# Kernel tuning notes

Hardware: AMD Instinct MI355X
Metric: run time of the kernel (lower is better)

The kernel has to match this reference:

```python
import jax, jax.numpy as jnp
import numpy as np

D_MODEL = 1024
D_STATE = 16
D_CONV = 4
EXPAND = 2
D_INNER = EXPAND * D_MODEL          # 2048
DT_RANK = (D_MODEL + 15) // 16      # 64 (mamba default 'auto')
B_SZ = 4
SEQ = 2048
EPS = 1e-12


def setup_inputs() -> dict:
    key = jax.random.key(0)
    ks = jax.random.split(key, 12)
    s = 0.02
    n = lambda k, sh: (jax.random.normal(k, sh, jnp.float32) * s)
    A_log = jnp.log(jnp.broadcast_to(
        jnp.arange(1, D_STATE + 1, dtype=jnp.float32), (D_INNER, D_STATE)))
    return {
        "input_tensor": jax.random.normal(ks[0], (B_SZ, SEQ, D_MODEL), jnp.float32),
        "in_proj_w": n(ks[1], (2 * D_INNER, D_MODEL)),
        "conv_w": n(ks[2], (D_INNER, D_CONV)),
        "conv_b": n(ks[3], (D_INNER,)),
        "x_proj_w": n(ks[4], (DT_RANK + 2 * D_STATE, D_INNER)),
        "dt_proj_w": n(ks[5], (D_INNER, DT_RANK)),
        "dt_proj_b": jax.random.uniform(ks[6], (D_INNER,), jnp.float32, -4.0, -2.0),
        "A_log": A_log,
        "D": jnp.ones((D_INNER,), jnp.float32),
        "out_proj_w": n(ks[7], (D_MODEL, D_INNER)),
        "norm_w": jnp.ones((D_MODEL,), jnp.float32),
        "ffn_w1": n(ks[8], (4 * D_MODEL, D_MODEL)),
        "ffn_b1": jnp.zeros((4 * D_MODEL,), jnp.float32),
        "ffn_w2": n(ks[9], (D_MODEL, 4 * D_MODEL)),
        "ffn_b2": jnp.zeros((D_MODEL,), jnp.float32),
        "ffn_norm_w": jnp.ones((D_MODEL,), jnp.float32),
    }


def rmsnorm(x, w, eps=EPS):
    return x * jax.lax.rsqrt(jnp.mean(x * x, axis=-1, keepdims=True) + eps) * w


def causal_dwconv(x, w, b):
    # x: (B, L, D); w: (D, K) depthwise causal conv, output length L
    xc = jnp.swapaxes(x, 1, 2)  # (B, D, L)
    out = jax.lax.conv_general_dilated(
        xc, w[:, None, :], window_strides=(1,),
        padding=[(w.shape[1] - 1, 0)],
        dimension_numbers=("NCH", "OIH", "NCH"),
        feature_group_count=w.shape[0])
    return jnp.swapaxes(out, 1, 2) + b


def selective_scan(u, delta, A, Bm, Cm):
    # u, delta: (B, L, D); Bm, Cm: (B, L, N); A: (D, N)
    def step(h, inp):
        d_t, u_t, b_t, c_t = inp           # (B,D), (B,D), (B,N), (B,N)
        dA = jnp.exp(d_t[..., None] * A)   # (B, D, N)
        h = dA * h + (d_t * u_t)[..., None] * b_t[:, None, :]
        y = jnp.einsum("bdn,bn->bd", h, c_t)
        return h, y
    h0 = jnp.zeros((u.shape[0], u.shape[2], A.shape[1]), u.dtype)
    xs = (jnp.swapaxes(delta, 0, 1), jnp.swapaxes(u, 0, 1),
          jnp.swapaxes(Bm, 0, 1), jnp.swapaxes(Cm, 0, 1))
    _, ys = jax.lax.scan(step, h0, xs)     # ys: (L, B, D)
    return jnp.swapaxes(ys, 0, 1)


def mamba_block(x, in_proj_w, conv_w, conv_b, x_proj_w, dt_proj_w, dt_proj_b,
                A_log, D, out_proj_w):
    xz = x @ in_proj_w.T                    # (B, L, 2*D_INNER)
    u, z = jnp.split(xz, 2, axis=-1)
    u = jax.nn.silu(causal_dwconv(u, conv_w, conv_b))
    x_dbl = u @ x_proj_w.T                  # (B, L, dt_rank + 2*N)
    dt = x_dbl[..., :DT_RANK]
    Bm = x_dbl[..., DT_RANK:DT_RANK + D_STATE]
    Cm = x_dbl[..., DT_RANK + D_STATE:]
    delta = jax.nn.softplus(dt @ dt_proj_w.T + dt_proj_b)
    A = -jnp.exp(A_log)
    y = selective_scan(u, delta, A, Bm, Cm) + u * D
    y = y * jax.nn.silu(z)
    return y @ out_proj_w.T


def reference(input_tensor, in_proj_w, conv_w, conv_b, x_proj_w, dt_proj_w,
              dt_proj_b, A_log, D, out_proj_w, norm_w, ffn_w1, ffn_b1,
              ffn_w2, ffn_b2, ffn_norm_w):
    h = mamba_block(input_tensor, in_proj_w, conv_w, conv_b, x_proj_w,
                    dt_proj_w, dt_proj_b, A_log, D, out_proj_w)
    # num_blocks=2 -> residual; dropout is identity at eval
    h = rmsnorm(h + input_tensor, norm_w)
    ff = jax.nn.gelu(h @ ffn_w1.T + ffn_b1, approximate=False) @ ffn_w2.T + ffn_b2
    return rmsnorm(ff + h, ffn_norm_w)
```

## Files before the change

kernel.cpp:

```cpp
#include <hip/hip_runtime.h>
#include <cstdint>
#include <cstddef>

#define SEQ    2048
#define NB     4
#define DM     1024
#define DI     2048
#define MTOK   (NB*SEQ)
#define NCHUNK 32
#define TCH    64

typedef unsigned short u16;
typedef __attribute__((ext_vector_type(8))) short  short8;
typedef __attribute__((ext_vector_type(4))) float  f32x4;
typedef __attribute__((ext_vector_type(4))) unsigned short us4;

__device__ __forceinline__ float b2f(u16 u){ union{unsigned i; float f;} c; c.i=((unsigned)u)<<16; return c.f; }
__device__ __forceinline__ u16 f2b(float f){
  union{float f; unsigned u;} c; c.f=f;
  unsigned r = c.u + 0x7fffu + ((c.u>>16)&1u);
  return (u16)(r>>16);
}

__device__ __forceinline__ void gload_lds16(const void* g, void* l){
  __builtin_amdgcn_global_load_lds((const __attribute__((address_space(1))) void*)g,
                                   (__attribute__((address_space(3))) void*)l, 16, 0, 0);
}

__global__ __launch_bounds__(256) void cvt_k(const float* __restrict__ in,
                                             u16* __restrict__ out, int n8){
  const int i = blockIdx.x*256 + threadIdx.x;
  if (i >= n8) return;
  const f32x4 a = ((const f32x4*)in)[2*i];
  const f32x4 b = ((const f32x4*)in)[2*i+1];
  short8 r;
  #pragma unroll
  for (int e=0;e<4;e++){ r[e] = (short)f2b(a[e]); r[e+4] = (short)f2b(b[e]); }
  ((short8*)out)[i] = r;
}

__global__ __launch_bounds__(256) void padcvt_k(const float* __restrict__ in,
                                                u16* __restrict__ out){
  const int i = blockIdx.x*256 + threadIdx.x;
  const int row = (i*8) >> 11;
  short8 r;
  if (row < 96){
    const f32x4 a = ((const f32x4*)in)[2*i];
    const f32x4 b = ((const f32x4*)in)[2*i+1];
    #pragma unroll
    for (int e=0;e<4;e++){ r[e] = (short)f2b(a[e]); r[e+4] = (short)f2b(b[e]); }
  } else {
    #pragma unroll
    for (int e=0;e<8;e++) r[e] = 0;
  }
  ((short8*)out)[i] = r;
}

template<int MW, int EPI>
__global__ __launch_bounds__(512, 2) void gemm8(
    const u16* __restrict__ X, int lda,
    const u16* __restrict__ W,
    const float* __restrict__ bias,
    void* __restrict__ Cout,
    int N, int K, int gridX)
{
  constexpr int BM = 128*MW;
  __shared__ __align__(16) u16 As[2][MW][128*64];
  __shared__ __align__(16) u16 Bs[2][2][128*64];

  const int nwg  = gridDim.x;
  const int orig = blockIdx.x;
  const int swz  = (orig & 7)*(nwg >> 3) + (orig >> 3);
  const int bm0  = (swz / gridX) * BM;
  const int bn0  = (swz % gridX) * 256;

  const int tid  = threadIdx.x;
  const int lane = tid & 63;
  const int wv   = tid >> 6;
  const int wm   = wv >> 2;
  const int wn   = wv & 3;

  const int trow = tid >> 3;
  const int sl   = tid & 7;
  const int scol = (sl ^ (trow & 7)) << 3;

  const u16* gA = X + (size_t)bm0*lda + scol;
  const u16* gB = W + (size_t)bn0*K   + scol;
  const int nk = K >> 6;

  auto stageA = [&](int slot, int unit, int tile){
    if (tile < nk){
      const int kt = tile << 6;
      #pragma unroll
      for (int l=0;l<2;l++){
        const int hrow = l*64 + trow;
        gload_lds16(gA + (size_t)(unit*128 + hrow)*lda + kt,
                    &As[slot][unit][hrow*64 + sl*8]);
      }
    }
  };
  auto stageB = [&](int slot, int half, int tile){
    if (tile < nk){
      const int kt = tile << 6;
      #pragma unroll
      for (int l=0;l<2;l++){
        const int hrow = l*64 + trow;
        gload_lds16(gB + (size_t)(half*128 + hrow)*K + kt,
                    &Bs[slot][half][hrow*64 + sl*8]);
      }
    }
  };

  f32x4 acc[4][MW][4];
  #pragma unroll
  for (int p=0;p<4;p++)
    #pragma unroll
    for (int i=0;i<MW;i++)
      #pragma unroll
      for (int j=0;j<4;j++){ f32x4 z={0.f,0.f,0.f,0.f}; acc[p][i][j]=z; }

  const int lrow = lane & 15;
  const int lhi  = lane >> 4;
  const int r7   = lane & 7;

  stageB(0,0,0); stageB(0,1,0);
  stageA(0,0,0); if constexpr (MW==2) stageA(0,1,0);
  stageB(1,0,1); stageB(1,1,1);
  if constexpr (MW==2) stageA(1,0,1);
  if constexpr (MW==2) asm volatile("s_waitcnt vmcnt(6)":::"memory");
  else                 asm volatile("s_waitcnt vmcnt(4)":::"memory");
  __builtin_amdgcn_s_barrier();

  for (int T0 = 0; T0 < nk; T0 += 2) {
    #pragma unroll
    for (int sub = 0; sub < 2; ++sub) {
      const int T = T0 + sub;
      short8 bf[4][2];
      #pragma unroll
      for (int p = 0; p < 4; ++p) {
        if (p == 0) {
          #pragma unroll
          for (int j=0;j<4;j++){
            const int gn = wn*64 + j*16 + lrow;
            const int bh = gn >> 7, br = gn & 127;
            #pragma unroll
            for (int ks=0;ks<2;ks++){
              const int s8 = ((ks<<2)|lhi) ^ r7;
              bf[j][ks] = *(const short8*)&Bs[sub][bh][br*64 + s8*8];
            }
          }
        }
        short8 af[MW][2];
        #pragma unroll
        for (int i=0;i<MW;i++){
          const int gm = (2*p + wm)*(16*MW) + i*16 + lrow;
          const int ah = (MW==2) ? (gm >> 7) : 0;
          const int ar = gm & 127;
          #pragma unroll
          for (int ks=0;ks<2;ks++){
            const int s8 = ((ks<<2)|lhi) ^ r7;
            af[i][ks] = *(const short8*)&As[sub][ah][ar*64 + s8*8];
          }
        }
        if (p == 0)      stageA(sub^1, MW-1, T+1);
        else if (p == 1) stageB(sub, 0, T+2);
        else if (p == 2) stageB(sub, 1, T+2);
        else if constexpr (MW==2) { if (p == 3) stageA(sub, 0, T+2); }
        if (p == 3 && T+1 < nk) {
          if (T+2 < nk) {
            if constexpr (MW==2) asm volatile("s_waitcnt vmcnt(6)":::"memory");
            else                 asm volatile("s_waitcnt vmcnt(4)":::"memory");
          } else {
            asm volatile("s_waitcnt vmcnt(0)":::"memory");
          }
        }
        __builtin_amdgcn_s_barrier();
        asm volatile("s_waitcnt lgkmcnt(0)":::"memory");
        __builtin_amdgcn_s_setprio(1);
        #pragma unroll
        for (int ks=0;ks<2;ks++)
          #pragma unroll
          for (int i=0;i<MW;i++)
            #pragma unroll
            for (int j=0;j<4;j++)
              acc[p][i][j] = __builtin_amdgcn_mfma_f32_16x16x32_bf16(af[i][ks], bf[j][ks], acc[p][i][j], 0, 0, 0);
        __builtin_amdgcn_s_setprio(0);
        __builtin_amdgcn_s_barrier();
      }
    }
  }

  const int r0 = (lane >> 4) << 2;
  #pragma unroll
  for (int p=0;p<4;p++){
    #pragma unroll
    for (int i=0;i<MW;i++){
      #pragma unroll
      for (int j=0;j<4;j++){
        const int col = bn0 + wn*64 + j*16 + lrow;
        float bval = 0.f;
        if constexpr (EPI >= 2) bval = bias[col];
        #pragma unroll
        for (int r=0;r<4;r++){
          const int row = bm0 + (2*p + wm)*(16*MW) + i*16 + r0 + r;
          const float v = acc[p][i][j][r];
          const size_t oid = (size_t)row*N + col;
          if constexpr (EPI == 0) {
            ((u16*)Cout)[oid] = f2b(v);
          } else if constexpr (EPI == 1) {
            ((float*)Cout)[oid] = v;
          } else if constexpr (EPI == 2) {
            float xv = v + bval;
            float sp = (xv > 20.f) ? xv : log1pf(__expf(xv));
            ((u16*)Cout)[oid] = f2b(sp);
          } else if constexpr (EPI == 3) {
            float xv = v + bval;
            float g = 0.5f*xv*(1.f + erff(xv*0.70710678118f));
            ((u16*)Cout)[oid] = f2b(g);
          } else {
            ((float*)Cout)[oid] = v + bval;
          }
        }
      }
    }
  }
}

template<int EPI>
__global__ __launch_bounds__(256) void gemm_bt(
    const u16* __restrict__ X, int lda,
    const u16* __restrict__ W,
    const float* __restrict__ bias,
    void* __restrict__ Cout,
    int M, int N, int K)
{
  __shared__ __align__(16) u16 As[128*64];
  __shared__ __align__(16) u16 Bs[128*64];
  const int tid  = threadIdx.x;
  const int lane = tid & 63;
  const int wv   = tid >> 6;
  const int wr   = wv >> 1, wc = wv & 1;
  const int bm0  = blockIdx.y * 128;
  const int bn0  = blockIdx.x * 128;
  const int r0   = tid >> 3;
  const int c8   = (tid & 7) << 3;

  f32x4 acc[4][4];
  #pragma unroll
  for (int i=0;i<4;i++)
    #pragma unroll
    for (int j=0;j<4;j++){ f32x4 z = {0.f,0.f,0.f,0.f}; acc[i][j] = z; }

  const int lrow = lane & 15;
  const int lko  = (lane >> 4) << 3;

  for (int kt = 0; kt < K; kt += 64) {
    #pragma unroll
    for (int c = 0; c < 4; ++c) {
      const int row = c*32 + r0;
      gload_lds16(X + (size_t)(bm0+row)*lda + kt + c8, &As[row*64 + c8]);
      gload_lds16(W + (size_t)(bn0+row)*K   + kt + c8, &Bs[row*64 + c8]);
    }
    __syncthreads();
    #pragma unroll
    for (int kk = 0; kk < 2; ++kk) {
      short8 af[4], bf[4];
      #pragma unroll
      for (int i=0;i<4;i++) af[i] = *(const short8*)&As[(wr*64 + i*16 + lrow)*64 + kk*32 + lko];
      #pragma unroll
      for (int j=0;j<4;j++) bf[j] = *(const short8*)&Bs[(wc*64 + j*16 + lrow)*64 + kk*32 + lko];
      #pragma unroll
      for (int i=0;i<4;i++)
        #pragma unroll
        for (int j=0;j<4;j++)
          acc[i][j] = __builtin_amdgcn_mfma_f32_16x16x32_bf16(af[i], bf[j], acc[i][j], 0, 0, 0);
    }
    __syncthreads();
  }

  const int rbase = bm0 + wr*64 + ((lane>>4)<<2);
  const int cbase = bn0 + wc*64 + (lane & 15);
  #pragma unroll
  for (int i=0;i<4;i++) {
    #pragma unroll
    for (int j=0;j<4;j++) {
      const int col = cbase + j*16;
      float bval = 0.f;
      if constexpr (EPI >= 2) bval = bias[col];
      #pragma unroll
      for (int r=0;r<4;r++) {
        const int row = rbase + i*16 + r;
        const float v = acc[i][j][r];
        const size_t oid = (size_t)row*N + col;
        if constexpr (EPI == 0) {
          ((u16*)Cout)[oid] = f2b(v);
        } else if constexpr (EPI == 1) {
          ((float*)Cout)[oid] = v;
        } else if constexpr (EPI == 2) {
          float xv = v + bval;
          float sp = (xv > 20.f) ? xv : log1pf(__expf(xv));
          ((u16*)Cout)[oid] = f2b(sp);
        } else if constexpr (EPI == 3) {
          float xv = v + bval;
          float g = 0.5f*xv*(1.f + erff(xv*0.70710678118f));
          ((u16*)Cout)[oid] = f2b(g);
        } else {
          ((float*)Cout)[oid] = v + bval;
        }
      }
    }
  }
}

__global__ __launch_bounds__(256) void gemm_thin(
    const u16* __restrict__ X, int lda,
    const u16* __restrict__ W,
    u16* __restrict__ Cout, int K)
{
  __shared__ __align__(16) u16 As[32*64];
  __shared__ __align__(16) u16 Bs[128*64];
  const int tid  = threadIdx.x;
  const int lane = tid & 63;
  const int wvq  = tid >> 6;
  const int bm0  = blockIdx.x * 32;
  const int srow = tid >> 3;
  const int c8   = (tid & 7) << 3;

  f32x4 acc[2][2];
  #pragma unroll
  for (int i=0;i<2;i++)
    #pragma unroll
    for (int j=0;j<2;j++){ f32x4 z={0.f,0.f,0.f,0.f}; acc[i][j]=z; }

  const int lrow = lane & 15;
  const int lko  = (lane >> 4) << 3;

  for (int kt = 0; kt < K; kt += 64) {
    gload_lds16(X + (size_t)(bm0+srow)*lda + kt + c8, &As[srow*64 + c8]);
    #pragma unroll
    for (int c=0;c<4;c++){
      const int row = c*32 + srow;
      gload_lds16(W + (size_t)row*K + kt + c8, &Bs[row*64 + c8]);
    }
    __syncthreads();
    #pragma unroll
    for (int ks=0;ks<2;ks++){
      short8 af[2], bf[2];
      #pragma unroll
      for (int i=0;i<2;i++) af[i] = *(const short8*)&As[(i*16+lrow)*64 + ks*32 + lko];
      #pragma unroll
      for (int j=0;j<2;j++) bf[j] = *(const short8*)&Bs[(wvq*32 + j*16 + lrow)*64 + ks*32 + lko];
      #pragma unroll
      for (int i=0;i<2;i++)
        #pragma unroll
        for (int j=0;j<2;j++)
          acc[i][j] = __builtin_amdgcn_mfma_f32_16x16x32_bf16(af[i], bf[j], acc[i][j], 0, 0, 0);
    }
    __syncthreads();
  }

  const int r0 = (lane >> 4) << 2;
  #pragma unroll
  for (int i=0;i<2;i++)
    #pragma unroll
    for (int j=0;j<2;j++){
      const int col = wvq*32 + j*16 + lrow;
      #pragma unroll
      for (int r=0;r<4;r++){
        const int row = bm0 + i*16 + r0 + r;
        Cout[(size_t)row*128 + col] = f2b(acc[i][j][r]);
      }
    }
}

__global__ __launch_bounds__(256) void conv_silu_k(
    const u16* __restrict__ xz, const float* __restrict__ cw,
    const float* __restrict__ cb, u16* __restrict__ uout)
{
  const int m0 = blockIdx.x << 2;
  const int t0 = m0 & (SEQ-1);
  const int d8 = threadIdx.x << 3;
  float w[4][8];
  const float* wp = cw + (size_t)d8*4;
  #pragma unroll
  for (int q=0;q<8;q++){
    f32x4 v = ((const f32x4*)wp)[q];
    #pragma unroll
    for (int e=0;e<4;e++){ int li=q*4+e; w[li&3][li>>2]=v[e]; }
  }
  float bias[8];
  {
    f32x4 b0 = ((const f32x4*)&cb[d8])[0];
    f32x4 b1 = ((const f32x4*)&cb[d8])[1];
    #pragma unroll
    for (int e=0;e<4;e++){ bias[e]=b0[e]; bias[e+4]=b1[e]; }
  }
  float xv[7][8];
  #pragma unroll
  for (int r=0;r<7;r++){
    const int t = t0 - 3 + r;
    if (t >= 0){
      short8 v = *(const short8*)&xz[(size_t)(m0-3+r)*4096 + d8];
      #pragma unroll
      for (int e=0;e<8;e++) xv[r][e] = b2f((u16)v[e]);
    } else {
      #pragma unroll
      for (int e=0;e<8;e++) xv[r][e] = 0.f;
    }
  }
  #pragma unroll
  for (int q=0;q<4;q++){
    short8 r8;
    #pragma unroll
    for (int e=0;e<8;e++){
      float a = bias[e];
      #pragma unroll
      for (int j=0;j<4;j++) a = fmaf(xv[q+j][e], w[j][e], a);
      r8[e] = (short)f2b(a / (1.f + __expf(-a)));
    }
    *(short8*)&uout[(size_t)(m0+q)*2048 + d8] = r8;
  }
}

template<int PASS>
__global__ __launch_bounds__(256) void scan_chunk_k(
    u16* __restrict__ dly,
    const u16* __restrict__ ucv,
    const u16* __restrict__ xz,
    const u16* __restrict__ xdbl,
    const float* __restrict__ A_log,
    const float* __restrict__ Dp,
    float* __restrict__ summ)
{
  __shared__ __align__(16) u16 sBC [TCH*32];
  __shared__ __align__(16) u16 sDel[16*256];
  __shared__ __align__(16) u16 sU  [16*256];
  __shared__ __align__(16) u16 sZ  [16*256];

  const int tid   = threadIdx.x;
  const int chgrp = blockIdx.x;
  const int chunk = blockIdx.y;
  const int ch    = chgrp*256 + tid;
  const int b     = ch >> 11;
  const int d     = ch & (DI-1);
  const int t0    = chunk*TCH;
  const int dbase = (chgrp & 7) << 8;

  float A[16];
  #pragma unroll
  for (int n=0;n<16;n++) A[n] = -__expf(A_log[d*16 + n]);

  {
    const int row = tid >> 2, q8 = (tid & 3) << 3;
    *(short8*)&sBC[row*32 + q8] =
      *(const short8*)&xdbl[((size_t)(b*SEQ) + t0 + row)*128 + 64 + q8];
  }

  float h[16];
  if constexpr (PASS == 1) {
    #pragma unroll
    for (int n=0;n<16;n++) h[n] = 0.f;
  } else {
    #pragma unroll
    for (int n=0;n<16;n++) h[n] = summ[((size_t)(chunk*17 + n))*8192 + ch];
  }
  float S = 0.f;
  float Dd = 0.f;
  if constexpr (PASS == 3) Dd = Dp[d];

  const int srow = tid >> 5;
  const int scol = (tid & 31) << 3;
  const size_t gD = (size_t)(b*SEQ)*DI   + dbase + scol;
  const size_t gZ = (size_t)(b*SEQ)*4096 + 2048 + dbase + scol;

  short8 pD[2], pU[2], pZ[2];
  #pragma unroll
  for (int k=0;k<2;k++){
    const size_t tg = (size_t)(t0 + k*8 + srow);
    pD[k] = *(const short8*)&dly[gD + tg*DI];
    pU[k] = *(const short8*)&ucv[gD + tg*DI];
    if constexpr (PASS == 3) pZ[k] = *(const short8*)&xz[gZ + tg*4096];
  }

  for (int sc = 0; sc < TCH/16; ++sc) {
    __syncthreads();
    #pragma unroll
    for (int k=0;k<2;k++){
      *(short8*)&sDel[(k*8+srow)*256 + scol] = pD[k];
      *(short8*)&sU  [(k*8+srow)*256 + scol] = pU[k];
      if constexpr (PASS == 3) *(short8*)&sZ[(k*8+srow)*256 + scol] = pZ[k];
    }
    if (sc < TCH/16 - 1) {
      #pragma unroll
      for (int k=0;k<2;k++){
        const size_t tg = (size_t)(t0 + (sc+1)*16 + k*8 + srow);
        pD[k] = *(const short8*)&dly[gD + tg*DI];
        pU[k] = *(const short8*)&ucv[gD + tg*DI];
        if constexpr (PASS == 3) pZ[k] = *(const short8*)&xz[gZ + tg*4096];
      }
    }
    __syncthreads();

    #pragma unroll 2
    for (int j=0; j<16; ++j){
      const int r = sc*16 + j;
      const float del = b2f(sDel[j*256 + tid]);
      const float u   = b2f(sU  [j*256 + tid]);
      const float du  = del * u;
      if constexpr (PASS == 1) S += del;
      const short8 bv0 = *(const short8*)&sBC[r*32];
      const short8 bv1 = *(const short8*)&sBC[r*32 + 8];
      short8 cv0, cv1;
      if constexpr (PASS == 3){
        cv0 = *(const short8*)&sBC[r*32 + 16];
        cv1 = *(const short8*)&sBC[r*32 + 24];
      }
      float p0=0.f, p1=0.f, p2=0.f, p3=0.f;
      #pragma unroll
      for (int n=0;n<16;++n){
        const float Bn = b2f((u16)(n<8 ? bv0[n] : bv1[n-8]));
        const float eA = __expf(del * A[n]);
        h[n] = fmaf(eA, h[n], du * Bn);
        if constexpr (PASS == 3){
          const float Cn = b2f((u16)(n<8 ? cv0[n] : cv1[n-8]));
          if      ((n&3)==0) p0 = fmaf(h[n], Cn, p0);
          else if ((n&3)==1) p1 = fmaf(h[n], Cn, p1);
          else if ((n&3)==2) p2 = fmaf(h[n], Cn, p2);
          else               p3 = fmaf(h[n], Cn, p3);
        }
      }
      if constexpr (PASS == 3){
        const float p = (p0+p1)+(p2+p3);
        const float z = b2f(sZ[j*256 + tid]);
        float y = fmaf(u, Dd, p);
        y *= z / (1.f + __expf(-z));
        dly[(size_t)(b*SEQ + t0 + r)*DI + d] = f2b(y);
      }
    }
  }

  if constexpr (PASS == 1){
    #pragma unroll
    for (int n=0;n<16;n++) summ[((size_t)(chunk*17 + n))*8192 + ch] = h[n];
    summ[((size_t)(chunk*17 + 16))*8192 + ch] = S;
  }
}

__global__ __launch_bounds__(256) void scan_combine_k(
    float* __restrict__ summ, const float* __restrict__ A_log)
{
  const int ch = blockIdx.x*256 + threadIdx.x;
  const int d  = ch & (DI-1);
  float A[16];
  #pragma unroll
  for (int n=0;n<16;n++) A[n] = -__expf(A_log[d*16 + n]);
  float hi[16];
  #pragma unroll
  for (int n=0;n<16;n++) hi[n] = 0.f;
  for (int c=0; c<NCHUNK; ++c){
    float hf[16]; float Sc = 0.f;
    if (c < NCHUNK-1) {
      #pragma unroll
      for (int n=0;n<16;n++) hf[n] = summ[((size_t)(c*17 + n))*8192 + ch];
      Sc = summ[((size_t)(c*17 + 16))*8192 + ch];
    }
    #pragma unroll
    for (int n=0;n<16;n++) summ[((size_t)(c*17 + n))*8192 + ch] = hi[n];
    if (c < NCHUNK-1) {
      #pragma unroll
      for (int n=0;n<16;n++) hi[n] = fmaf(__expf(A[n]*Sc), hi[n], hf[n]);
    }
  }
}

template<bool RES_BF, bool OUT_BF>
__global__ __launch_bounds__(256) void add_rms_k(
    const float* __restrict__ a, const void* __restrict__ res,
    const float* __restrict__ wgt, void* __restrict__ out)
{
  const int row = blockIdx.x;
  const int tid = threadIdx.x;
  const size_t base = (size_t)row*DM + tid*4;
  const f32x4 av = *(const f32x4*)&a[base];
  const f32x4 wv = *(const f32x4*)&wgt[tid*4];
  float v[4]; float ss = 0.f;
  if constexpr (RES_BF) {
    const us4 rv = *(const us4*)&((const u16*)res)[base];
    #pragma unroll
    for (int j=0;j<4;j++){ v[j] = av[j] + b2f(rv[j]); ss = fmaf(v[j], v[j], ss); }
  } else {
    const f32x4 rv = *(const f32x4*)&((const float*)res)[base];
    #pragma unroll
    for (int j=0;j<4;j++){ v[j] = av[j] + rv[j]; ss = fmaf(v[j], v[j], ss); }
  }
  #pragma unroll
  for (int off=32; off>=1; off>>=1) ss += __shfl_xor(ss, off);
  __shared__ float sred[4];
  if ((tid & 63) == 0) sred[tid>>6] = ss;
  __syncthreads();
  const float tot = sred[0]+sred[1]+sred[2]+sred[3];
  const float rs = rsqrtf(tot * (1.f/1024.f) + 1e-12f);
  if constexpr (OUT_BF) {
    us4 ov;
    #pragma unroll
    for (int j=0;j<4;j++) ov[j] = (unsigned short)f2b(v[j] * rs * wv[j]);
    *(us4*)&((u16*)out)[base] = ov;
  } else {
    f32x4 ov;
    #pragma unroll
    for (int j=0;j<4;j++) ov[j] = v[j] * rs * wv[j];
    *(f32x4*)&((float*)out)[base] = ov;
  }
}

extern "C" void kernel_launch(void* const* d_in, const int* in_sizes, int n_in,
                              void* d_out, int out_size, void* d_ws, size_t ws_size,
                              hipStream_t stream) {
  (void)in_sizes; (void)n_in; (void)out_size; (void)ws_size;
  const float* x_in  = (const float*)d_in[0];
  const float* w_inp = (const float*)d_in[1];
  const float* conv_w= (const float*)d_in[2];
  const float* conv_b= (const float*)d_in[3];
  const float* w_xp  = (const float*)d_in[4];
  const float* w_dt  = (const float*)d_in[5];
  const float* b_dt  = (const float*)d_in[6];
  const float* A_log = (const float*)d_in[7];
  const float* Dp    = (const float*)d_in[8];
  const float* w_out = (const float*)d_in[9];
  const float* norm_w= (const float*)d_in[10];
  const float* w_f1  = (const float*)d_in[11];
  const float* b_f1  = (const float*)d_in[12];
  const float* w_f2  = (const float*)d_in[13];
  const float* b_f2  = (const float*)d_in[14];
  const float* norm2 = (const float*)d_in[15];

  char* ws = (char*)d_ws;
  size_t off = 0;
  auto alloc = [&](size_t bytes){ void* p = ws + off; off += (bytes + 255) & ~255ull; return p; };
  u16*   xz   = (u16*)  alloc((size_t)MTOK*4096*2);
  u16*   ucv  = (u16*)  alloc((size_t)MTOK*2048*2);
  u16*   xdbl = (u16*)  alloc((size_t)MTOK*128*2);
  u16*   dly  = (u16*)  alloc((size_t)MTOK*2048*2);
  float* tmp  = (float*)alloc((size_t)MTOK*1024*4);
  u16*   wA   = (u16*)  alloc((size_t)4096*1024*2);
  u16*   wpad = (u16*)  alloc((size_t)128*2048*2);
  u16*   wdt  = (u16*)  alloc((size_t)2048*64*2);
  u16*   wout = (u16*)  alloc((size_t)1024*2048*2);
  u16*   xbf  = (u16*)tmp;
  float* summ = tmp;
  u16*   hbuf = ucv;

  cvt_k<<<4096, 256, 0, stream>>>(x_in,  xbf, MTOK*DM/8);
  cvt_k<<<2048, 256, 0, stream>>>(w_inp, wA,  (2*DI*DM)/8);
  padcvt_k<<<128, 256, 0, stream>>>(w_xp, wpad);
  cvt_k<<<64,   256, 0, stream>>>(w_dt,  wdt, (DI*64)/8);
  cvt_k<<<1024, 256, 0, stream>>>(w_out, wout,(DM*DI)/8);

  gemm8<2,0><<<512, 512, 0, stream>>>(xbf, 1024, wA, nullptr, xz, 4096, 1024, 16);
  conv_silu_k<<<MTOK/4, 256, 0, stream>>>(xz, conv_w, conv_b, ucv);
  gemm_thin<<<256, 256, 0, stream>>>(ucv, 2048, wpad, xdbl, 2048);
  gemm_bt<2><<<dim3(16,64), 256, 0, stream>>>(xdbl, 128, wdt, b_dt, dly, MTOK, 2048, 64);
  scan_chunk_k<1><<<dim3(32, NCHUNK-1), 256, 0, stream>>>(dly, ucv, xz, xdbl, A_log, Dp, summ);
  scan_combine_k<<<32, 256, 0, stream>>>(summ, A_log);
  scan_chunk_k<3><<<dim3(32, NCHUNK), 256, 0, stream>>>(dly, ucv, xz, xdbl, A_log, Dp, summ);
  gemm8<1,1><<<256, 512, 0, stream>>>(dly, 2048, wout, nullptr, tmp, 1024, 2048, 4);
  add_rms_k<false,true><<<MTOK, 256, 0, stream>>>(tmp, x_in, norm_w, hbuf);
  cvt_k<<<2048, 256, 0, stream>>>(w_f1, wA, (4*DM*DM)/8);
  gemm8<2,3><<<512, 512, 0, stream>>>(hbuf, 1024, wA, b_f1, xz, 4096, 1024, 16);
  cvt_k<<<2048, 256, 0, stream>>>(w_f2, wA, (4*DM*DM)/8);
  gemm8<1,4><<<256, 512, 0, stream>>>(xz, 4096, wA, b_f2, tmp, 1024, 4096, 4);
  add_rms_k<true,false><<<MTOK, 256, 0, stream>>>(tmp, hbuf, norm2, d_out);
}
```

Measured before the change: 622.5 us.

## Replace large 8-wave GEMM with simpler 128x128 double-buffered GEMM; merge conversion kernels

Replaces the 256x256/128x256 tile, 512-thread GEMM, which had a fine-grained interleaved prefetch schedule, with a 128x128 tile, 256-thread kernel that uses plain double buffering and one barrier pair per k-tile. It also fuses the five fp32-to-bf16 conversion launches into one kernel that dispatches on block index. The simpler GEMM launches more blocks with smaller tiles, which cuts per-block register and LDS pressure. In exchange each tile gets less data reuse and there is more global/LDS traffic per FLOP, and the loss of the tuned overlap schedule risks lower MFMA utilisation.

```diff
diff --git a/kernel.cpp b/kernel.cpp
--- a/kernel.cpp
+++ b/kernel.cpp
@@ -27,6 +27,44 @@
                                    (__attribute__((address_space(3))) void*)l, 16, 0, 0);
 }
 
+__global__ __launch_bounds__(256) void mega_cvt(
+    const float* __restrict__ x,    const float* __restrict__ winp,
+    const float* __restrict__ wxp,  const float* __restrict__ wdt_,
+    const float* __restrict__ wout_,
+    u16* __restrict__ xbf, u16* __restrict__ wA, u16* __restrict__ wpadb,
+    u16* __restrict__ wdtb, u16* __restrict__ woutb)
+{
+  const int b = blockIdx.x;
+  const int t = threadIdx.x;
+  const float* src; u16* dst; int i;
+  if (b < 4096)      { i = b*256 + t;        src = x;     dst = xbf;  }
+  else if (b < 6144) { i = (b-4096)*256 + t; src = winp;  dst = wA;   }
+  else if (b < 6272) {
+    i = (b-6144)*256 + t;
+    const int row = (i*8) >> 11;
+    short8 r;
+    if (row < 96){
+      const f32x4 a = ((const f32x4*)wxp)[2*i];
+      const f32x4 c = ((const f32x4*)wxp)[2*i+1];
+      #pragma unroll
+      for (int e=0;e<4;e++){ r[e]=(short)f2b(a[e]); r[e+4]=(short)f2b(c[e]); }
+    } else {
+      #pragma unroll
+      for (int e=0;e<8;e++) r[e]=0;
+    }
+    ((short8*)wpadb)[i] = r;
+    return;
+  }
+  else if (b < 6336) { i = (b-6272)*256 + t; src = wdt_;  dst = wdtb; }
+  else               { i = (b-6336)*256 + t; src = wout_; dst = woutb;}
+  const f32x4 a = ((const f32x4*)src)[2*i];
+  const f32x4 c = ((const f32x4*)src)[2*i+1];
+  short8 r;
+  #pragma unroll
+  for (int e=0;e<4;e++){ r[e]=(short)f2b(a[e]); r[e+4]=(short)f2b(c[e]); }
+  ((short8*)dst)[i] = r;
+}
+
 __global__ __launch_bounds__(256) void cvt_k(const float* __restrict__ in,
                                              u16* __restrict__ out, int n8){
   const int i = blockIdx.x*256 + threadIdx.x;
@@ -39,46 +77,27 @@
   ((short8*)out)[i] = r;
 }
 
-__global__ __launch_bounds__(256) void padcvt_k(const float* __restrict__ in,
-                                                u16* __restrict__ out){
-  const int i = blockIdx.x*256 + threadIdx.x;
-  const int row = (i*8) >> 11;
-  short8 r;
-  if (row < 96){
-    const f32x4 a = ((const f32x4*)in)[2*i];
-    const f32x4 b = ((const f32x4*)in)[2*i+1];
-    #pragma unroll
-    for (int e=0;e<4;e++){ r[e] = (short)f2b(a[e]); r[e+4] = (short)f2b(b[e]); }
-  } else {
-    #pragma unroll
-    for (int e=0;e<8;e++) r[e] = 0;
-  }
-  ((short8*)out)[i] = r;
-}
-
-template<int MW, int EPI>
-__global__ __launch_bounds__(512, 2) void gemm8(
+template<int EPI>
+__global__ __launch_bounds__(256, 2) void gemm_db(
     const u16* __restrict__ X, int lda,
     const u16* __restrict__ W,
     const float* __restrict__ bias,
     void* __restrict__ Cout,
     int N, int K, int gridX)
 {
-  constexpr int BM = 128*MW;
-  __shared__ __align__(16) u16 As[2][MW][128*64];
-  __shared__ __align__(16) u16 Bs[2][2][128*64];
+  __shared__ __align__(16) u16 Ab[2][128*64];
+  __shared__ __align__(16) u16 Bb[2][128*64];
 
   const int nwg  = gridDim.x;
   const int orig = blockIdx.x;
   const int swz  = (orig & 7)*(nwg >> 3) + (orig >> 3);
-  const int bm0  = (swz / gridX) * BM;
-  const int bn0  = (swz % gridX) * 256;
+  const int bm0  = (swz / gridX) * 128;
+  const int bn0  = (swz % gridX) * 128;
 
   const int tid  = threadIdx.x;
   const int lane = tid & 63;
   const int wv   = tid >> 6;
-  const int wm   = wv >> 2;
-  const int wn   = wv & 3;
+  const int wr   = wv >> 1, wc = wv & 1;
 
   const int trow = tid >> 3;
   const int sl   = tid & 7;
@@ -88,138 +107,88 @@
   const u16* gB = W + (size_t)bn0*K   + scol;
   const int nk = K >> 6;
 
-  auto stageA = [&](int slot, int unit, int tile){
-    if (tile < nk){
-      const int kt = tile << 6;
-      #pragma unroll
-      for (int l=0;l<2;l++){
-        const int hrow = l*64 + trow;
-        gload_lds16(gA + (size_t)(unit*128 + hrow)*lda + kt,
-                    &As[slot][unit][hrow*64 + sl*8]);
-      }
+  auto stage = [&](int buf, int tile){
+    const int kt = tile << 6;
+    #pragma unroll
+    for (int g=0; g<4; ++g){
+      const int row = g*32 + trow;
+      gload_lds16(gA + (size_t)row*lda + kt, &Ab[buf][row*64 + sl*8]);
+    }
+    #pragma unroll
+    for (int g=0; g<4; ++g){
+      const int row = g*32 + trow;
+      gload_lds16(gB + (size_t)row*K + kt, &Bb[buf][row*64 + sl*8]);
     }
   };
-  auto stageB = [&](int slot, int half, int tile){
-    if (tile < nk){
-      const int kt = tile << 6;
-      #pragma unroll
-      for (int l=0;l<2;l++){
-        const int hrow = l*64 + trow;
-        gload_lds16(gB + (size_t)(half*128 + hrow)*K + kt,
-                    &Bs[slot][half][hrow*64 + sl*8]);
-      }
-    }
-  };
-
-  f32x4 acc[4][MW][4];
-  #pragma unroll
-  for (int p=0;p<4;p++)
-    #pragma unroll
-    for (int i=0;i<MW;i++)
-      #pragma unroll
-      for (int j=0;j<4;j++){ f32x4 z={0.f,0.f,0.f,0.f}; acc[p][i][j]=z; }
+
+  f32x4 acc[4][4];
+  #pragma unroll
+  for (int i=0;i<4;i++)
+    #pragma unroll
+    for (int j=0;j<4;j++){ f32x4 z={0.f,0.f,0.f,0.f}; acc[i][j]=z; }
 
   const int lrow = lane & 15;
   const int lhi  = lane >> 4;
   const int r7   = lane & 7;
 
-  stageB(0,0,0); stageB(0,1,0);
-  stageA(0,0,0); if constexpr (MW==2) stageA(0,1,0);
-  stageB(1,0,1); stageB(1,1,1);
-  if constexpr (MW==2) stageA(1,0,1);
-  if constexpr (MW==2) asm volatile("s_waitcnt vmcnt(6)":::"memory");
-  else                 asm volatile("s_waitcnt vmcnt(4)":::"memory");
-  __builtin_amdgcn_s_barrier();
-
-  for (int T0 = 0; T0 < nk; T0 += 2) {
-    #pragma unroll
-    for (int sub = 0; sub < 2; ++sub) {
-      const int T = T0 + sub;
-      short8 bf[4][2];
-      #pragma unroll
-      for (int p = 0; p < 4; ++p) {
-        if (p == 0) {
-          #pragma unroll
-          for (int j=0;j<4;j++){
-            const int gn = wn*64 + j*16 + lrow;
-            const int bh = gn >> 7, br = gn & 127;
-            #pragma unroll
-            for (int ks=0;ks<2;ks++){
-              const int s8 = ((ks<<2)|lhi) ^ r7;
-              bf[j][ks] = *(const short8*)&Bs[sub][bh][br*64 + s8*8];
-            }
-          }
-        }
-        short8 af[MW][2];
+  stage(0, 0);
+  stage(1, 1);
+
+  for (int t = 0; t < nk; ++t) {
+    if (t + 1 < nk) asm volatile("s_waitcnt vmcnt(8)":::"memory");
+    else            asm volatile("s_waitcnt vmcnt(0)":::"memory");
+    __builtin_amdgcn_s_barrier();
+    {
+      const u16* As = Ab[t&1];
+      const u16* Bs = Bb[t&1];
+      #pragma unroll
+      for (int ks=0; ks<2; ++ks){
+        const int s8 = ((ks<<2)|lhi) ^ r7;
+        short8 af[4], bf[4];
         #pragma unroll
-        for (int i=0;i<MW;i++){
-          const int gm = (2*p + wm)*(16*MW) + i*16 + lrow;
-          const int ah = (MW==2) ? (gm >> 7) : 0;
-          const int ar = gm & 127;
-          #pragma unroll
-          for (int ks=0;ks<2;ks++){
-            const int s8 = ((ks<<2)|lhi) ^ r7;
-            af[i][ks] = *(const short8*)&As[sub][ah][ar*64 + s8*8];
-          }
-        }
-        if (p == 0)      stageA(sub^1, MW-1, T+1);
-        else if (p == 1) stageB(sub, 0, T+2);
-        else if (p == 2) stageB(sub, 1, T+2);
-        else if constexpr (MW==2) { if (p == 3) stageA(sub, 0, T+2); }
-        if (p == 3 && T+1 < nk) {
-          if (T+2 < nk) {
-            if constexpr (MW==2) asm volatile("s_waitcnt vmcnt(6)":::"memory");
-            else                 asm volatile("s_waitcnt vmcnt(4)":::"memory");
-          } else {
-            asm volatile("s_waitcnt vmcnt(0)":::"memory");
-          }
-        }
-        __builtin_amdgcn_s_barrier();
-        asm volatile("s_waitcnt lgkmcnt(0)":::"memory");
+        for (int i=0;i<4;i++) af[i] = *(const short8*)&As[(wr*64 + i*16 + lrow)*64 + s8*8];
+        #pragma unroll
+        for (int j=0;j<4;j++) bf[j] = *(const short8*)&Bs[(wc*64 + j*16 + lrow)*64 + s8*8];
         __builtin_amdgcn_s_setprio(1);
         #pragma unroll
-        for (int ks=0;ks<2;ks++)
+        for (int i=0;i<4;i++)
           #pragma unroll
-          for (int i=0;i<MW;i++)
-            #pragma unroll
-            for (int j=0;j<4;j++)
-              acc[p][i][j] = __builtin_amdgcn_mfma_f32_16x16x32_bf16(af[i][ks], bf[j][ks], acc[p][i][j], 0, 0, 0);
+          for (int j=0;j<4;j++)
+            acc[i][j] = __builtin_amdgcn_mfma_f32_16x16x32_bf16(af[i], bf[j], acc[i][j], 0, 0, 0);
         __builtin_amdgcn_s_setprio(0);
-        __builtin_amdgcn_s_barrier();
-      }
-    }
+      }
+    }
+    __builtin_amdgcn_s_barrier();
+    if (t + 2 < nk) stage(t&1, t+2);
   }
 
   const int r0 = (lane >> 4) << 2;
   #pragma unroll
-  for (int p=0;p<4;p++){
-    #pragma unroll
-    for (int i=0;i<MW;i++){
-      #pragma unroll
-      for (int j=0;j<4;j++){
-        const int col = bn0 + wn*64 + j*16 + lrow;
-        float bval = 0.f;
-        if constexpr (EPI >= 2) bval = bias[col];
-        #pragma unroll
-        for (int r=0;r<4;r++){
-          const int row = bm0 + (2*p + wm)*(16*MW) + i*16 + r0 + r;
-          const float v = acc[p][i][j][r];
-          const size_t oid = (size_t)row*N + col;
-          if constexpr (EPI == 0) {
-            ((u16*)Cout)[oid] = f2b(v);
-          } else if constexpr (EPI == 1) {
-            ((float*)Cout)[oid] = v;
-          } else if constexpr (EPI == 2) {
-            float xv = v + bval;
-            float sp = (xv > 20.f) ? xv : log1pf(__expf(xv));
-            ((u16*)Cout)[oid] = f2b(sp);
-          } else if constexpr (EPI == 3) {
-            float xv = v + bval;
-            float g = 0.5f*xv*(1.f + erff(xv*0.70710678118f));
-            ((u16*)Cout)[oid] = f2b(g);
-          } else {
-            ((float*)Cout)[oid] = v + bval;
-          }
+  for (int i=0;i<4;i++){
+    #pragma unroll
+    for (int j=0;j<4;j++){
+      const int col = bn0 + wc*64 + j*16 + lrow;
+      float bval = 0.f;
+      if constexpr (EPI >= 2) bval = bias[col];
+      #pragma unroll
+      for (int r=0;r<4;r++){
+        const int row = bm0 + wr*64 + i*16 + r0 + r;
+        const float v = acc[i][j][r];
+        const size_t oid = (size_t)row*N + col;
+        if constexpr (EPI == 0) {
+          ((u16*)Cout)[oid] = f2b(v);
+        } else if constexpr (EPI == 1) {
+          ((float*)Cout)[oid] = v;
+        } else if constexpr (EPI == 2) {
+          float xv = v + bval;
+          float sp = (xv > 20.f) ? xv : log1pf(__expf(xv));
+          ((u16*)Cout)[oid] = f2b(sp);
+        } else if constexpr (EPI == 3) {
+          float xv = v + bval;
+          float g = 0.5f*xv*(1.f + erff(xv*0.70710678118f));
+          ((u16*)Cout)[oid] = f2b(g);
+        } else {
+          ((float*)Cout)[oid] = v + bval;
         }
       }
     }
@@ -650,24 +619,21 @@
   float* summ = tmp;
   u16*   hbuf = ucv;
 
-  cvt_k<<<4096, 256, 0, stream>>>(x_in,  xbf, MTOK*DM/8);
-  cvt_k<<<2048, 256, 0, stream>>>(w_inp, wA,  (2*DI*DM)/8);
-  padcvt_k<<<128, 256, 0, stream>>>(w_xp, wpad);
-  cvt_k<<<64,   256, 0, stream>>>(w_dt,  wdt, (DI*64)/8);
-  cvt_k<<<1024, 256, 0, stream>>>(w_out, wout,(DM*DI)/8);
-
-  gemm8<2,0><<<512, 512, 0, stream>>>(xbf, 1024, wA, nullptr, xz, 4096, 1024, 16);
+  mega_cvt<<<7360, 256, 0, stream>>>(x_in, w_inp, w_xp, w_dt, w_out,
+                                     xbf, wA, wpad, wdt, wout);
+
+  gemm_db<0><<<2048, 256, 0, stream>>>(xbf, 1024, wA, nullptr, xz, 4096, 1024, 32);
   conv_silu_k<<<MTOK/4, 256, 0, stream>>>(xz, conv_w, conv_b, ucv);
   gemm_thin<<<256, 256, 0, stream>>>(ucv, 2048, wpad, xdbl, 2048);
   gemm_bt<2><<<dim3(16,64), 256, 0, stream>>>(xdbl, 128, wdt, b_dt, dly, MTOK, 2048, 64);
   scan_chunk_k<1><<<dim3(32, NCHUNK-1), 256, 0, stream>>>(dly, ucv, xz, xdbl, A_log, Dp, summ);
   scan_combine_k<<<32, 256, 0, stream>>>(summ, A_log);
   scan_chunk_k<3><<<dim3(32, NCHUNK), 256, 0, stream>>>(dly, ucv, xz, xdbl, A_log, Dp, summ);
-  gemm8<1,1><<<256, 512, 0, stream>>>(dly, 2048, wout, nullptr, tmp, 1024, 2048, 4);
+  gemm_db<1><<<512, 256, 0, stream>>>(dly, 2048, wout, nullptr, tmp, 1024, 2048, 8);
   add_rms_k<false,true><<<MTOK, 256, 0, stream>>>(tmp, x_in, norm_w, hbuf);
   cvt_k<<<2048, 256, 0, stream>>>(w_f1, wA, (4*DM*DM)/8);
-  gemm8<2,3><<<512, 512, 0, stream>>>(hbuf, 1024, wA, b_f1, xz, 4096, 1024, 16);
+  gemm_db<3><<<2048, 256, 0, stream>>>(hbuf, 1024, wA, b_f1, xz, 4096, 1024, 32);
   cvt_k<<<2048, 256, 0, stream>>>(w_f2, wA, (4*DM*DM)/8);
-  gemm8<1,4><<<256, 512, 0, stream>>>(xz, 4096, wA, b_f2, tmp, 1024, 4096, 4);
+  gemm_db<4><<<512, 256, 0, stream>>>(xz, 4096, wA, b_f2, tmp, 1024, 4096, 8);
   add_rms_k<true,false><<<MTOK, 256, 0, stream>>>(tmp, hbuf, norm2, d_out);
 }
```

Measured after the change: 617.5 us. No clear change (-0.8%).
